# Optimization experiments

Hardware: AMD Instinct MI355X
Metric: run time of the kernel (lower is better)

The kernel has to match this reference:

```python
import jax, jax.numpy as jnp
import numpy as np

# Module hyperparameters (from init_kwargs)
HEAD_DIM = 64
PX = 16          # patches_x
PY = 16          # patches_y
FREQ_BASE = 100.0
FREQ_SCALE = 1.0


def _precompute_coeffs(positions):
    """RoPE cos/sin tables for one axis. feat_dim = HEAD_DIM // 2."""
    feat_dim = HEAD_DIM // 2          # each block-diagonal block is head_dim/2 wide
    num_freqs = feat_dim // 2         # rope splits block into (x, y) halves
    freqs = FREQ_SCALE * FREQ_BASE ** (-jnp.arange(num_freqs, dtype=jnp.float32) / num_freqs)
    angles = positions.astype(jnp.float32)[:, None] * freqs[None, :]   # [Sp, num_freqs]
    return jnp.cos(angles), jnp.sin(angles)


def _rope_apply(feats, cos, sin, inverse=False):
    """feats: [B, H, S, D] with D == 2*cos.shape[-1]; cos/sin: [Sp, D//2], tiled to S."""
    S = feats.shape[2]
    rep = S // cos.shape[0]           # tile per-image coeffs across cameras
    cos = jnp.tile(cos, (rep, 1))[None, None]   # [1,1,S,D//2]
    sin = jnp.tile(sin, (rep, 1))[None, None]
    d = feats.shape[-1] // 2
    x_in, y_in = feats[..., :d], feats[..., d:]
    if inverse:
        return jnp.concatenate([cos * x_in - sin * y_in, sin * x_in + cos * y_in], axis=-1)
    return jnp.concatenate([cos * x_in + sin * y_in, -sin * x_in + cos * y_in], axis=-1)


def _block_diag_rope(feats, cx, sx, cy, sy, inverse=False):
    """Block-diagonal: first head_dim//2 dims get x-axis RoPE, second half get y-axis RoPE."""
    h = feats.shape[-1] // 2
    return jnp.concatenate([
        _rope_apply(feats[..., :h], cx, sx, inverse),
        _rope_apply(feats[..., h:], cy, sy, inverse),
    ], axis=-1)


def setup_inputs() -> dict:
    key = jax.random.key(0)
    kq, kk, kv, kvm, kks = jax.random.split(key, 5)
    B, H, CAM = 2, 16, 8
    S = CAM * PX * PY   # 2048
    q = jax.random.normal(kq, (B, H, S, HEAD_DIM), dtype=jnp.float32)
    k = jax.random.normal(kk, (B, H, S, HEAD_DIM), dtype=jnp.float32)
    v = jax.random.normal(kv, (B, H, S, HEAD_DIM), dtype=jnp.float32)
    viewmats = jax.random.normal(kvm, (B, CAM, 4, 4), dtype=jnp.float32)
    Ks = jax.random.normal(kks, (B, CAM, 3, 3), dtype=jnp.float32)
    return {"q": q, "k": k, "v": v, "viewmats": viewmats, "Ks": Ks}


def reference(q, k, v, viewmats, Ks):
    # Per-image patch-grid positions, 'split' ordering: x fastest.
    pos_x = jnp.tile(jnp.arange(PX), PY)               # [PX*PY]
    pos_y = jnp.repeat(jnp.arange(PY), PX)             # [PX*PY]
    cx, sx = _precompute_coeffs(pos_x)
    cy, sy = _precompute_coeffs(pos_y)

    qe = _block_diag_rope(q, cx, sx, cy, sy)
    ke = _block_diag_rope(k, cx, sx, cy, sy)
    ve = _block_diag_rope(v, cx, sx, cy, sy)

    scale = 1.0 / jnp.sqrt(jnp.asarray(q.shape[-1], dtype=q.dtype))
    logits = jnp.einsum('bhqd,bhkd->bhqk', qe, ke) * scale
    attn = jax.nn.softmax(logits, axis=-1)
    out = jnp.einsum('bhqk,bhkd->bhqd', attn, ve)

    # Inverse RoPE on the output (PRoPE epilogue).
    return _block_diag_rope(out, cx, sx, cy, sy, inverse=True)
```

## Files before the change

### kernel.cpp

```cpp
#include <hip/hip_runtime.h>
#include <stdint.h>
#include <math.h>

typedef __attribute__((ext_vector_type(8))) short bf16x8;
typedef __attribute__((ext_vector_type(16))) float f32x16;

#define S_LEN 2048
#define D_HEAD 64
#define NT 32
#define TILE_USH 4096
#define SCALE_LOG2E 0.1803368801111204f

static __device__ __forceinline__ unsigned short f2bf(float f) {
    union { float f; uint32_t u; } v; v.f = f;
    return (unsigned short)((v.u + 0x7fffu + ((v.u >> 16) & 1u)) >> 16);
}
static __device__ __forceinline__ uint32_t cvtpk(float lo, float hi) {
    uint32_t r;
    asm("v_cvt_pk_bf16_f32 %0, %1, %2" : "=v"(r) : "v"(lo), "v"(hi));
    return r;
}
static __device__ __forceinline__ float exp2_fast(float x) {
    float r;
    asm("v_exp_f32 %0, %1" : "=v"(r) : "v"(x));
    return r;
}
static __device__ __forceinline__ void pswap(uint32_t& a, uint32_t& b) {
    asm("v_permlane32_swap_b32 %0, %1" : "+v"(a), "+v"(b));
}

static __device__ __forceinline__ void build_tables(float (*tc)[16][16], float (*ts)[16][16], int tid) {
    for (int e = tid; e < 512; e += 256) {
        int axis = e >> 8, pp = (e >> 4) & 15, j = e & 15;
        float freq = powf(100.0f, -(float)j * (1.0f / 16.0f));
        float ang = (float)pp * freq;
        float sv, cv;
        sincosf(ang, &sv, &cv);
        tc[axis][pp][j] = cv;
        ts[axis][pp][j] = sv;
    }
}

static __device__ __forceinline__ void rope_chunk(const float* __restrict__ src, int row0, int r, int c,
                                                  const float (*tc)[16][16], const float (*ts)[16][16],
                                                  float* e1, float* e2) {
    int d0 = c * 4;
    int srow = row0 + r;
    const float* p = src + (size_t)srow * D_HEAD + d0;
    float4 xv = *(const float4*)p;
    float4 yv = *(const float4*)(p + 16);
    float xs[4] = {xv.x, xv.y, xv.z, xv.w};
    float ys[4] = {yv.x, yv.y, yv.z, yv.w};
    int pos = srow & 255;
    int axis = c >> 3;
    int pp = axis ? (pos >> 4) : (pos & 15);
    int jb = d0 & 15;
#pragma unroll
    for (int i = 0; i < 4; ++i) {
        float cc = tc[axis][pp][jb + i];
        float ss = ts[axis][pp][jb + i];
        e1[i] = cc * xs[i] + ss * ys[i];
        e2[i] = cc * ys[i] - ss * xs[i];
    }
}

__global__ __launch_bounds__(256) void xyrope_prep_kernel(
    const float* __restrict__ k, const float* __restrict__ v,
    unsigned short* __restrict__ kw, unsigned short* __restrict__ vtw) {
    __shared__ unsigned short Kt[64][72];
    __shared__ unsigned short Vt[64][72];
    __shared__ float tc[2][16][16], ts[2][16][16];
    int tid = threadIdx.x;
    build_tables(tc, ts, tid);
    __syncthreads();

    int bid = blockIdx.x;
    int bh = bid >> 5, kt = bid & 31;
    const float* kh = k + (size_t)bh * S_LEN * D_HEAD;
    const float* vh = v + (size_t)bh * S_LEN * D_HEAD;
    unsigned short* kimg = kw + ((size_t)bh * NT + kt) * TILE_USH;
    unsigned short* vimg = vtw + ((size_t)bh * NT + kt) * TILE_USH;

#pragma unroll
    for (int half = 0; half < 2; ++half) {
        int r = (tid >> 3) + half * 32;
        int ci_ = tid & 7;
        int c = ci_ + ((ci_ >> 2) << 2);
        int d0 = c * 4;
        float e1[4], e2[4];
        rope_chunk(kh, kt * 64, r, c, tc, ts, e1, e2);
#pragma unroll
        for (int i = 0; i < 4; ++i) { Kt[r][d0 + i] = f2bf(e1[i]); Kt[r][d0 + 16 + i] = f2bf(e2[i]); }
        rope_chunk(vh, kt * 64, r, c, tc, ts, e1, e2);
#pragma unroll
        for (int i = 0; i < 4; ++i) { Vt[r][d0 + i] = f2bf(e1[i]); Vt[r][d0 + 16 + i] = f2bf(e2[i]); }
    }
    __syncthreads();

    int l = tid & 63, grp = tid >> 6;
#pragma unroll
    for (int half = 0; half < 2; ++half) {
        int ci = grp + half * 4;
        int mt = ci & 1, ks = ci >> 1;
        {
            int row = (l & 31) + 32 * mt;
            int d0 = (l >> 5) * 8 + 16 * ks;
            uint4 w = *(const uint4*)&Kt[row][d0];
            *(uint4*)(kimg + ci * 512 + l * 8) = w;
        }
        {
            int dcol = (l & 31) + 32 * mt;
            int k0 = (l >> 5) * 8 + 16 * ks;
            union { unsigned short u[8]; uint4 q; } ov;
#pragma unroll
            for (int j = 0; j < 8; ++j) ov.u[j] = Vt[k0 + j][dcol];
            *(uint4*)(vimg + ci * 512 + l * 8) = ov.q;
        }
    }
}

struct AttnSmem {
    unsigned short Kb[2][TILE_USH];
    unsigned short Vb[2][TILE_USH];
    float tc[2][16][16];
    float ts[2][16][16];
};

static __device__ __forceinline__ void gl16(const void* g, void* l) {
    __builtin_amdgcn_global_load_lds((const __attribute__((address_space(1))) unsigned int*)g,
                                     (__attribute__((address_space(3))) unsigned int*)l, 16, 0, 0);
}
static __device__ __forceinline__ void stage_tile(const unsigned short* img, unsigned short* dstbuf, int tid) {
    const char* src = (const char*)img + tid * 16;
    char* dst = (char*)dstbuf + (tid >> 6) * 1024;
    gl16(src, dst);
    gl16(src + 4096, dst + 4096);
}
static __device__ __forceinline__ bf16x8 frag_ld(const unsigned short* buf, int ci, int lane) {
    union { uint4 u; bf16x8 v; } c;
    c.u = *(const uint4*)(buf + ci * 512 + lane * 8);
    return c.v;
}

__global__ __launch_bounds__(256, 2) void xyrope_attn_kernel(
    const float* __restrict__ q, const unsigned short* __restrict__ kw,
    const unsigned short* __restrict__ vtw, float* __restrict__ out) {
    __shared__ AttnSmem sm;
    int tid = threadIdx.x, bid = blockIdx.x;

    int xcd = bid & 7, slot = bid >> 3;
    int bh = xcd * 4 + (slot >> 4);
    int qt = slot & 15;

    const unsigned short* kimg = kw + (size_t)bh * NT * TILE_USH;
    const unsigned short* vimg = vtw + (size_t)bh * NT * TILE_USH;

    build_tables(sm.tc, sm.ts, tid);
    stage_tile(kimg, sm.Kb[0], tid);
    stage_tile(vimg, sm.Vb[0], tid);
    __syncthreads();

    int lane = tid & 63, wave = tid >> 6;
    int ql = lane & 31, h = lane >> 5;
    int qrow = qt * 128 + wave * 32 + ql;
    int pos = qrow & 255, px = pos & 15, py = pos >> 4;

    const float* qp = q + ((size_t)bh * S_LEN + qrow) * D_HEAD + h * 8;
    float e[4][8];
#pragma unroll
    for (int ck = 0; ck < 4; ++ck) {
        float4 a = *(const float4*)(qp + ck * 16);
        float4 b = *(const float4*)(qp + ck * 16 + 4);
        e[ck][0] = a.x; e[ck][1] = a.y; e[ck][2] = a.z; e[ck][3] = a.w;
        e[ck][4] = b.x; e[ck][5] = b.y; e[ck][6] = b.z; e[ck][7] = b.w;
    }
#pragma unroll
    for (int ax = 0; ax < 2; ++ax) {
        int pp = ax ? py : px;
#pragma unroll
        for (int i = 0; i < 8; ++i) {
            float cc = sm.tc[ax][pp][8 * h + i];
            float ss = sm.ts[ax][pp][8 * h + i];
            float x = e[ax * 2][i], y = e[ax * 2 + 1][i];
            e[ax * 2][i] = (cc * x + ss * y) * SCALE_LOG2E;
            e[ax * 2 + 1][i] = (cc * y - ss * x) * SCALE_LOG2E;
        }
    }
    bf16x8 bq[4];
#pragma unroll
    for (int ck = 0; ck < 4; ++ck) {
        union { uint32_t w[4]; bf16x8 v; } u;
#pragma unroll
        for (int t = 0; t < 4; ++t) u.w[t] = cvtpk(e[ck][2 * t], e[ck][2 * t + 1]);
        bq[ck] = u.v;
    }

    float m_run = -INFINITY, l_run = 0.0f;
    f32x16 o0 = {}, o1 = {};

    for (int t = 0; t < NT; ++t) {
        int cur = t & 1;
        if (t + 1 < NT) {
            stage_tile(kimg + (t + 1) * TILE_USH, sm.Kb[cur ^ 1], tid);
            stage_tile(vimg + (t + 1) * TILE_USH, sm.Vb[cur ^ 1], tid);
        }
        const unsigned short* Ks = sm.Kb[cur];
        const unsigned short* Vs = sm.Vb[cur];

        f32x16 s0 = {}, s1 = {};
#pragma unroll
        for (int ks = 0; ks < 4; ++ks) {
            bf16x8 a0 = frag_ld(Ks, ks * 2 + 0, lane);
            bf16x8 a1 = frag_ld(Ks, ks * 2 + 1, lane);
            s0 = __builtin_amdgcn_mfma_f32_32x32x16_bf16(a0, bq[ks], s0, 0, 0, 0);
            s1 = __builtin_amdgcn_mfma_f32_32x32x16_bf16(a1, bq[ks], s1, 0, 0, 0);
        }

        float p[32];
#pragma unroll
        for (int r = 0; r < 16; ++r) { p[r] = s0[r]; p[16 + r] = s1[r]; }

        float t8[8];
#pragma unroll
        for (int i = 0; i < 8; ++i)
            t8[i] = fmaxf(fmaxf(p[i], p[i + 8]), fmaxf(p[i + 16], p[i + 24]));
        float pm = fmaxf(fmaxf(fmaxf(t8[0], t8[1]), fmaxf(t8[2], t8[3])),
                         fmaxf(fmaxf(t8[4], t8[5]), fmaxf(t8[6], t8[7])));
        pm = fmaxf(pm, __shfl_xor(pm, 32));

        if (!__all(pm <= m_run + 8.0f)) {
            float mn = fmaxf(m_run, pm);
            float al = exp2_fast(m_run - mn);
            o0 *= al; o1 *= al;
            l_run *= al;
            m_run = mn;
        }

#pragma unroll
        for (int i = 0; i < 32; ++i) p[i] = exp2_fast(p[i] - m_run);
        float a8[8];
#pragma unroll
        for (int i = 0; i < 8; ++i)
            a8[i] = (p[i] + p[i + 8]) + (p[i + 16] + p[i + 24]);
        float ps = ((a8[0] + a8[1]) + (a8[2] + a8[3])) + ((a8[4] + a8[5]) + (a8[6] + a8[7]));
        ps += __shfl_xor(ps, 32);
        l_run += ps;

        uint32_t pk[16];
#pragma unroll
        for (int tt = 0; tt < 16; ++tt) pk[tt] = cvtpk(p[2 * tt], p[2 * tt + 1]);

#pragma unroll
        for (int ks = 0; ks < 4; ++ks) {
            uint32_t w0 = pk[4 * ks], w1 = pk[4 * ks + 1], w2 = pk[4 * ks + 2], w3 = pk[4 * ks + 3];
            pswap(w0, w2);
            pswap(w1, w3);
            union { uint32_t w[4]; bf16x8 v; } pb;
            pb.w[0] = w0; pb.w[1] = w1; pb.w[2] = w2; pb.w[3] = w3;
            bf16x8 v0 = frag_ld(Vs, ks * 2 + 0, lane);
            bf16x8 v1 = frag_ld(Vs, ks * 2 + 1, lane);
            o0 = __builtin_amdgcn_mfma_f32_32x32x16_bf16(v0, pb.v, o0, 0, 0, 0);
            o1 = __builtin_amdgcn_mfma_f32_32x32x16_bf16(v1, pb.v, o1, 0, 0, 0);
        }
        __syncthreads();
    }

    float inv_l = 1.0f / l_run;
    float* orow = out + ((size_t)bh * S_LEN + qrow) * D_HEAD;
#pragma unroll
    for (int mt = 0; mt < 2; ++mt) {
        float oo[16];
#pragma unroll
        for (int r = 0; r < 16; ++r) oo[r] = mt ? o1[r] : o0[r];
        int pp = mt ? py : px;
        float res[16];
#pragma unroll
        for (int r = 0; r < 8; ++r) {
            int j = (r & 3) + 8 * (r >> 2) + 4 * h;
            float cc = sm.tc[mt][pp][j];
            float ss = sm.ts[mt][pp][j];
            float x = oo[r] * inv_l, y = oo[r + 8] * inv_l;
            res[r] = cc * x - ss * y;
            res[r + 8] = ss * x + cc * y;
        }
#pragma unroll
        for (int gq = 0; gq < 4; ++gq) {
            float4 w = {res[gq * 4 + 0], res[gq * 4 + 1], res[gq * 4 + 2], res[gq * 4 + 3]};
            *(float4*)(orow + mt * 32 + gq * 8 + 4 * h) = w;
        }
    }
}

extern "C" void kernel_launch(void* const* d_in, const int* in_sizes, int n_in,
                              void* d_out, int out_size, void* d_ws, size_t ws_size,
                              hipStream_t stream) {
    const float* q = (const float*)d_in[0];
    const float* k = (const float*)d_in[1];
    const float* v = (const float*)d_in[2];
    float* out = (float*)d_out;
    unsigned short* kw = (unsigned short*)d_ws;
    unsigned short* vtw = kw + (size_t)32 * NT * TILE_USH;
    hipLaunchKernelGGL(xyrope_prep_kernel, dim3(1024), dim3(256), 0, stream, k, v, kw, vtw);
    hipLaunchKernelGGL(xyrope_attn_kernel, dim3(512), dim3(256), 0, stream, q, kw, vtw, out);
}
```

Measured before the change: 76.80 us.

## Split KV sequence across two wave groups per block and merge softmax states

Doubles the block to 512 threads so two groups of four waves each process half the KV tiles for the same query rows, each with its own double-buffered LDS staging. At the end, group 1 writes its partial output, max and sum to a shared-memory area that reuses the tile buffers, and group 0 merges the two online-softmax states and applies the inverse RoPE epilogue. This aims to raise the number of active waves and halve the serial KV loop length, which matters because 512 blocks give little occupancy on the device. In exchange it uses twice the LDS per block, which limits how many blocks fit per CU, and adds a merge step plus a barrier.

Measured after the change: 70.05 us. 1.1x faster.

```diff
diff --git a/kernel.cpp b/kernel.cpp
--- a/kernel.cpp
+++ b/kernel.cpp
@@ -8,6 +8,7 @@
 #define S_LEN 2048
 #define D_HEAD 64
 #define NT 32
+#define NT_HALF 16
 #define TILE_USH 4096
 #define SCALE_LOG2E 0.1803368801111204f
 
@@ -29,8 +30,9 @@
     asm("v_permlane32_swap_b32 %0, %1" : "+v"(a), "+v"(b));
 }
 
-static __device__ __forceinline__ void build_tables(float (*tc)[16][16], float (*ts)[16][16], int tid) {
-    for (int e = tid; e < 512; e += 256) {
+static __device__ __forceinline__ void build_tables(float (*tc)[16][16], float (*ts)[16][16],
+                                                    int tid, int nthr) {
+    for (int e = tid; e < 512; e += nthr) {
         int axis = e >> 8, pp = (e >> 4) & 15, j = e & 15;
         float freq = powf(100.0f, -(float)j * (1.0f / 16.0f));
         float ang = (float)pp * freq;
@@ -71,7 +73,7 @@
     __shared__ unsigned short Vt[64][72];
     __shared__ float tc[2][16][16], ts[2][16][16];
     int tid = threadIdx.x;
-    build_tables(tc, ts, tid);
+    build_tables(tc, ts, tid, 256);
     __syncthreads();
 
     int bid = blockIdx.x;
@@ -120,8 +122,13 @@
 }
 
 struct AttnSmem {
-    unsigned short Kb[2][TILE_USH];
-    unsigned short Vb[2][TILE_USH];
+    union {
+        struct {
+            unsigned short Kb[2][2][TILE_USH];
+            unsigned short Vb[2][2][TILE_USH];
+        } b;
+        float mrg[4][64][34];
+    } u;
     float tc[2][16][16];
     float ts[2][16][16];
 };
@@ -130,9 +137,9 @@
     __builtin_amdgcn_global_load_lds((const __attribute__((address_space(1))) unsigned int*)g,
                                      (__attribute__((address_space(3))) unsigned int*)l, 16, 0, 0);
 }
-static __device__ __forceinline__ void stage_tile(const unsigned short* img, unsigned short* dstbuf, int tid) {
-    const char* src = (const char*)img + tid * 16;
-    char* dst = (char*)dstbuf + (tid >> 6) * 1024;
+static __device__ __forceinline__ void stage_tile(const unsigned short* img, unsigned short* dstbuf, int t256) {
+    const char* src = (const char*)img + t256 * 16;
+    char* dst = (char*)dstbuf + (t256 >> 6) * 1024;
     gl16(src, dst);
     gl16(src + 4096, dst + 4096);
 }
@@ -142,7 +149,7 @@
     return c.v;
 }
 
-__global__ __launch_bounds__(256, 2) void xyrope_attn_kernel(
+__global__ __launch_bounds__(512, 4) void xyrope_attn_kernel(
     const float* __restrict__ q, const unsigned short* __restrict__ kw,
     const unsigned short* __restrict__ vtw, float* __restrict__ out) {
     __shared__ AttnSmem sm;
@@ -152,15 +159,18 @@
     int bh = xcd * 4 + (slot >> 4);
     int qt = slot & 15;
 
-    const unsigned short* kimg = kw + (size_t)bh * NT * TILE_USH;
-    const unsigned short* vimg = vtw + (size_t)bh * NT * TILE_USH;
-
-    build_tables(sm.tc, sm.ts, tid);
-    stage_tile(kimg, sm.Kb[0], tid);
-    stage_tile(vimg, sm.Vb[0], tid);
+    int grp = tid >> 8;
+    int t256 = tid & 255;
+    const unsigned short* kimg = kw + ((size_t)bh * NT + grp * NT_HALF) * TILE_USH;
+    const unsigned short* vimg = vtw + ((size_t)bh * NT + grp * NT_HALF) * TILE_USH;
+
+    build_tables(sm.tc, sm.ts, tid, 512);
+    stage_tile(kimg, sm.u.b.Kb[grp][0], t256);
+    stage_tile(vimg, sm.u.b.Vb[grp][0], t256);
     __syncthreads();
 
-    int lane = tid & 63, wave = tid >> 6;
+    int lane = tid & 63;
+    int wave = (tid >> 6) & 3;
     int ql = lane & 31, h = lane >> 5;
     int qrow = qt * 128 + wave * 32 + ql;
     int pos = qrow & 255, px = pos & 15, py = pos >> 4;
@@ -189,23 +199,23 @@
     bf16x8 bq[4];
 #pragma unroll
     for (int ck = 0; ck < 4; ++ck) {
-        union { uint32_t w[4]; bf16x8 v; } u;
-#pragma unroll
-        for (int t = 0; t < 4; ++t) u.w[t] = cvtpk(e[ck][2 * t], e[ck][2 * t + 1]);
-        bq[ck] = u.v;
+        union { uint32_t w[4]; bf16x8 v; } uu;
+#pragma unroll
+        for (int t = 0; t < 4; ++t) uu.w[t] = cvtpk(e[ck][2 * t], e[ck][2 * t + 1]);
+        bq[ck] = uu.v;
     }
 
     float m_run = -INFINITY, l_run = 0.0f;
     f32x16 o0 = {}, o1 = {};
 
-    for (int t = 0; t < NT; ++t) {
+    for (int t = 0; t < NT_HALF; ++t) {
         int cur = t & 1;
-        if (t + 1 < NT) {
-            stage_tile(kimg + (t + 1) * TILE_USH, sm.Kb[cur ^ 1], tid);
-            stage_tile(vimg + (t + 1) * TILE_USH, sm.Vb[cur ^ 1], tid);
-        }
-        const unsigned short* Ks = sm.Kb[cur];
-        const unsigned short* Vs = sm.Vb[cur];
+        if (t + 1 < NT_HALF) {
+            stage_tile(kimg + (t + 1) * TILE_USH, sm.u.b.Kb[grp][cur ^ 1], t256);
+            stage_tile(vimg + (t + 1) * TILE_USH, sm.u.b.Vb[grp][cur ^ 1], t256);
+        }
+        const unsigned short* Ks = sm.u.b.Kb[grp][cur];
+        const unsigned short* Vs = sm.u.b.Vb[grp][cur];
 
         f32x16 s0 = {}, s1 = {};
 #pragma unroll
@@ -265,28 +275,49 @@
         __syncthreads();
     }
 
-    float inv_l = 1.0f / l_run;
-    float* orow = out + ((size_t)bh * S_LEN + qrow) * D_HEAD;
-#pragma unroll
-    for (int mt = 0; mt < 2; ++mt) {
-        float oo[16];
-#pragma unroll
-        for (int r = 0; r < 16; ++r) oo[r] = mt ? o1[r] : o0[r];
-        int pp = mt ? py : px;
-        float res[16];
-#pragma unroll
-        for (int r = 0; r < 8; ++r) {
-            int j = (r & 3) + 8 * (r >> 2) + 4 * h;
-            float cc = sm.tc[mt][pp][j];
-            float ss = sm.ts[mt][pp][j];
-            float x = oo[r] * inv_l, y = oo[r + 8] * inv_l;
-            res[r] = cc * x - ss * y;
-            res[r + 8] = ss * x + cc * y;
-        }
-#pragma unroll
-        for (int gq = 0; gq < 4; ++gq) {
-            float4 w = {res[gq * 4 + 0], res[gq * 4 + 1], res[gq * 4 + 2], res[gq * 4 + 3]};
-            *(float4*)(orow + mt * 32 + gq * 8 + 4 * h) = w;
+    float* pl = &sm.u.mrg[wave][lane][0];
+    if (grp == 1) {
+#pragma unroll
+        for (int r = 0; r < 16; ++r) { pl[r] = o0[r]; pl[16 + r] = o1[r]; }
+        pl[32] = m_run;
+        pl[33] = l_run;
+    }
+    __syncthreads();
+    if (grp == 0) {
+        float mB = pl[32], lB = pl[33];
+        float mS = fmaxf(m_run, mB);
+        float a0 = exp2_fast(m_run - mS);
+        float a1 = exp2_fast(mB - mS);
+        float lt = l_run * a0 + lB * a1;
+        float inv_l = 1.0f / lt;
+#pragma unroll
+        for (int r = 0; r < 16; ++r) {
+            o0[r] = o0[r] * a0 + pl[r] * a1;
+            o1[r] = o1[r] * a0 + pl[16 + r] * a1;
+        }
+
+        float* orow = out + ((size_t)bh * S_LEN + qrow) * D_HEAD;
+#pragma unroll
+        for (int mt = 0; mt < 2; ++mt) {
+            float oo[16];
+#pragma unroll
+            for (int r = 0; r < 16; ++r) oo[r] = mt ? o1[r] : o0[r];
+            int pp = mt ? py : px;
+            float res[16];
+#pragma unroll
+            for (int r = 0; r < 8; ++r) {
+                int j = (r & 3) + 8 * (r >> 2) + 4 * h;
+                float cc = sm.tc[mt][pp][j];
+                float ss = sm.ts[mt][pp][j];
+                float x = oo[r] * inv_l, y = oo[r + 8] * inv_l;
+                res[r] = cc * x - ss * y;
+                res[r + 8] = ss * x + cc * y;
+            }
+#pragma unroll
+            for (int gq = 0; gq < 4; ++gq) {
+                float4 w = {res[gq * 4 + 0], res[gq * 4 + 1], res[gq * 4 + 2], res[gq * 4 + 3]};
+                *(float4*)(orow + mt * 32 + gq * 8 + 4 * h) = w;
+            }
         }
     }
 }
@@ -301,5 +332,5 @@
     unsigned short* kw = (unsigned short*)d_ws;
     unsigned short* vtw = kw + (size_t)32 * NT * TILE_USH;
     hipLaunchKernelGGL(xyrope_prep_kernel, dim3(1024), dim3(256), 0, stream, k, v, kw, vtw);
-    hipLaunchKernelGGL(xyrope_attn_kernel, dim3(512), dim3(256), 0, stream, q, kw, vtw, out);
-}
+    hipLaunchKernelGGL(xyrope_attn_kernel, dim3(512), dim3(512), 0, stream, q, kw, vtw, out);
+}
```
